# Performance work log

Measured on AMD Instinct MI355X. Metric: run time of the kernel, lower is better.

## Reference

```python
import jax, jax.numpy as jnp
import numpy as np

B, C, H, W = 64, 3, 512, 512


def setup_inputs() -> dict:
    key = jax.random.key(0)
    return {"segmentation_mask": jax.random.normal(key, (B, C, H, W), dtype=jnp.float32)}


def _vertical_height(pred_mask, label):
    # pred_mask: (B, H, W) int. Returns (B, 1) float32 = ymax - ymin for rows
    # containing `label`, or 0 if the label is absent (matches the torch loop
    # which leaves bounds at zeros).
    row_any = (pred_mask == label).any(axis=2)          # (B, H) bool
    has = row_any.any(axis=1)                            # (B,)
    Hdim = row_any.shape[1]
    ymin = jnp.argmax(row_any, axis=1)                   # first True row
    ymax = Hdim - 1 - jnp.argmax(row_any[:, ::-1], axis=1)  # last True row
    height = jnp.where(has, (ymax - ymin).astype(jnp.float32), 0.0)
    return height[:, None]                               # (B, 1)


def reference(segmentation_mask):
    pred_mask = jnp.argmax(segmentation_mask, axis=1)    # (B, H, W)

    cup_height = _vertical_height(pred_mask, 1)          # (B, 1)
    disc_height = _vertical_height(pred_mask, 2)         # (B, 1)
    cdr = cup_height / (disc_height + 1e-6)              # (B, 1)

    prob_map = jax.nn.softmax(segmentation_mask, axis=1) # (B, 3, H, W)
    cup_prob = prob_map[:, 1]                            # (B, H, W)
    disc_prob = prob_map[:, 2]

    # AdaptiveAvgPool2d(1)+Flatten on a (B,1,H,W) map == global spatial mean,
    # identical to .mean(dim=(1,2)); the original concatenates both, so the
    # disc/cup means appear twice.
    disc_mean = disc_prob.mean(axis=(1, 2))[:, None]     # (B, 1)
    cup_mean = cup_prob.mean(axis=(1, 2))[:, None]       # (B, 1)

    return jnp.concatenate([cdr, disc_mean, cup_mean, disc_mean, cup_mean], axis=1)  # (B, 5)
```

## Files before the change

### kernel.cpp

```cpp
#include <hip/hip_runtime.h>
#include <hip/hip_bf16.h>
#include <math.h>


#define BATCH 64
#define CHAN 3
#define HDIM 512
#define WDIM 512
#define HW (HDIM * WDIM)
#define RPB 8
#define THREADS 256
#define VECS_PER_ROW (WDIM / 4)
#define NV (RPB * VECS_PER_ROW)
#define ITERS (NV / THREADS)
#define NBLOCKS (BATCH * (HDIM / RPB))

typedef float vfloat4 __attribute__((ext_vector_type(4)));

struct Accum {
    int ymax1[BATCH];
    int yminenc1[BATCH];
    int ymax2[BATCH];
    int yminenc2[BATCH];
    float sum1[BATCH];
    float sum2[BATCH];
};

__global__ __launch_bounds__(THREADS) void cdr_main(const float* __restrict__ in,
                                                    Accum* __restrict__ acc) {
    const int b = blockIdx.x >> 6;
    const int chunk = blockIdx.x & 63;
    const int row0 = chunk * RPB;

    const vfloat4* __restrict__ c0 =
        (const vfloat4*)(in + (size_t)b * CHAN * HW + (size_t)row0 * WDIM);
    const vfloat4* __restrict__ c1 = c0 + (HW / 4);
    const vfloat4* __restrict__ c2 = c1 + (HW / 4);

    vfloat4 va[ITERS], vb[ITERS], vc[ITERS];
#pragma unroll
    for (int j = 0; j < ITERS; ++j) {
        const int v = threadIdx.x + j * THREADS;
        va[j] = __builtin_nontemporal_load(&c0[v]);
        vb[j] = __builtin_nontemporal_load(&c1[v]);
        vc[j] = __builtin_nontemporal_load(&c2[v]);
    }

    float acc1 = 0.0f, acc2 = 0.0f;
    unsigned m = 0u;
    const int rbase = threadIdx.x >> 7;

#pragma unroll
    for (int j = 0; j < ITERS; ++j) {
        unsigned f1 = 0u, f2 = 0u;

#define DO_PX(V0, V1, V2)                                        \
        {                                                        \
            f1 |= (unsigned)(((V1) > (V0)) & ((V1) >= (V2)));    \
            f2 |= (unsigned)(((V2) > (V0)) & ((V2) > (V1)));     \
            float e0 = __expf(V0);                               \
            float e1 = __expf(V1);                               \
            float e2 = __expf(V2);                               \
            float inv = __builtin_amdgcn_rcpf(e0 + e1 + e2);     \
            acc1 += e1 * inv;                                    \
            acc2 += e2 * inv;                                    \
        }

        DO_PX(va[j].x, vb[j].x, vc[j].x)
        DO_PX(va[j].y, vb[j].y, vc[j].y)
        DO_PX(va[j].z, vb[j].z, vc[j].z)
        DO_PX(va[j].w, vb[j].w, vc[j].w)
#undef DO_PX

        const int row = rbase + 2 * j;
        m |= (f1 << row) | (f2 << (16 + row));
    }

#pragma unroll
    for (int off = 32; off > 0; off >>= 1) {
        m |= __shfl_xor(m, off, 64);
        acc1 += __shfl_down(acc1, off, 64);
        acc2 += __shfl_down(acc2, off, 64);
    }

    __shared__ unsigned s_m[THREADS / 64];
    __shared__ float s_red1[THREADS / 64];
    __shared__ float s_red2[THREADS / 64];
    const int wave = threadIdx.x >> 6;
    if ((threadIdx.x & 63) == 0) {
        s_m[wave] = m;
        s_red1[wave] = acc1;
        s_red2[wave] = acc2;
    }
    __syncthreads();

    if (threadIdx.x == 0) {
        float t1 = 0.0f, t2 = 0.0f;
        unsigned mm = 0u;
        for (int w = 0; w < THREADS / 64; ++w) {
            t1 += s_red1[w];
            t2 += s_red2[w];
            mm |= s_m[w];
        }
        atomicAdd(&acc->sum1[b], t1);
        atomicAdd(&acc->sum2[b], t2);

        const unsigned bm1 = mm & 0xFFu;
        const unsigned bm2 = (mm >> 16) & 0xFFu;
        if (bm1) {
            const int bmin = row0 + (__ffs(bm1) - 1);
            const int bmax = row0 + (31 - __clz(bm1));
            atomicMax(&acc->ymax1[b], bmax);
            atomicMax(&acc->yminenc1[b], (HDIM - 1) - bmin);
        }
        if (bm2) {
            const int bmin = row0 + (__ffs(bm2) - 1);
            const int bmax = row0 + (31 - __clz(bm2));
            atomicMax(&acc->ymax2[b], bmax);
            atomicMax(&acc->yminenc2[b], (HDIM - 1) - bmin);
        }
    }
}

__global__ void cdr_finalize(const Accum* __restrict__ acc, float* __restrict__ out) {
    const int b = threadIdx.x;
    if (b < BATCH) {
        const int ymax1 = acc->ymax1[b];
        const int ymax2 = acc->ymax2[b];
        const int ymin1 = (HDIM - 1) - acc->yminenc1[b];
        const int ymin2 = (HDIM - 1) - acc->yminenc2[b];
        float h1 = (ymax1 >= 0) ? (float)(ymax1 - ymin1) : 0.0f;
        float h2 = (ymax2 >= 0) ? (float)(ymax2 - ymin2) : 0.0f;
        float cdr = h1 / (h2 + 1e-6f);
        const float inv_hw = 1.0f / (float)HW;
        float cup_mean = acc->sum1[b] * inv_hw;
        float disc_mean = acc->sum2[b] * inv_hw;
        out[b * 5 + 0] = cdr;
        out[b * 5 + 1] = disc_mean;
        out[b * 5 + 2] = cup_mean;
        out[b * 5 + 3] = disc_mean;
        out[b * 5 + 4] = cup_mean;
    }
}

extern "C" void kernel_launch(void* const* d_in, const int* in_sizes, int n_in,
                              void* d_out, int out_size, void* d_ws, size_t ws_size,
                              hipStream_t stream) {
    const float* in = (const float*)d_in[0];
    float* out = (float*)d_out;
    Accum* acc = (Accum*)d_ws;

    cdr_main<<<NBLOCKS, THREADS, 0, stream>>>(in, acc);
    cdr_finalize<<<1, 64, 0, stream>>>(acc, out);
}
```

Before: 266.7 us.

## Double-buffer register loads across row chunks with larger per-block work

Each block now covers 32 rows instead of 8, processed as four chunks with a register double buffer that prefetches the next chunk while computing the current one. Row masks for the two labels are split into separate 32-bit words. This aims to overlap memory latency with exp/compare work and to reduce block count and atomic traffic. It raises register pressure and lowers the number of blocks, which may hurt occupancy and latency hiding.

```diff
diff --git a/kernel.cpp b/kernel.cpp
--- a/kernel.cpp
+++ b/kernel.cpp
@@ -8,12 +8,11 @@
 #define HDIM 512
 #define WDIM 512
 #define HW (HDIM * WDIM)
-#define RPB 8
 #define THREADS 256
-#define VECS_PER_ROW (WDIM / 4)
-#define NV (RPB * VECS_PER_ROW)
-#define ITERS (NV / THREADS)
-#define NBLOCKS (BATCH * (HDIM / RPB))
+#define CHUNKS 4
+#define BLOCKS_PER_IMG 16
+#define NBLOCKS (BATCH * BLOCKS_PER_IMG)
+#define CHUNK_V 1024
 
 typedef float vfloat4 __attribute__((ext_vector_type(4)));
 
@@ -28,67 +27,82 @@
 
 __global__ __launch_bounds__(THREADS) void cdr_main(const float* __restrict__ in,
                                                     Accum* __restrict__ acc) {
-    const int b = blockIdx.x >> 6;
-    const int chunk = blockIdx.x & 63;
-    const int row0 = chunk * RPB;
+    const int b = blockIdx.x >> 4;
+    const int part = blockIdx.x & 15;
+    const int row0 = part * 32;
 
     const vfloat4* __restrict__ c0 =
         (const vfloat4*)(in + (size_t)b * CHAN * HW + (size_t)row0 * WDIM);
     const vfloat4* __restrict__ c1 = c0 + (HW / 4);
     const vfloat4* __restrict__ c2 = c1 + (HW / 4);
 
-    vfloat4 va[ITERS], vb[ITERS], vc[ITERS];
+    vfloat4 A[2][3][4];
+
+    auto load_chunk = [&](int c, int buf) {
 #pragma unroll
-    for (int j = 0; j < ITERS; ++j) {
-        const int v = threadIdx.x + j * THREADS;
-        va[j] = __builtin_nontemporal_load(&c0[v]);
-        vb[j] = __builtin_nontemporal_load(&c1[v]);
-        vc[j] = __builtin_nontemporal_load(&c2[v]);
-    }
+        for (int j = 0; j < 4; ++j) {
+            const int v = c * CHUNK_V + j * THREADS + (int)threadIdx.x;
+            A[buf][0][j] = __builtin_nontemporal_load(&c0[v]);
+            A[buf][1][j] = __builtin_nontemporal_load(&c1[v]);
+            A[buf][2][j] = __builtin_nontemporal_load(&c2[v]);
+        }
+    };
+
+    load_chunk(0, 0);
 
     float acc1 = 0.0f, acc2 = 0.0f;
-    unsigned m = 0u;
+    unsigned m1 = 0u, m2 = 0u;
     const int rbase = threadIdx.x >> 7;
 
 #pragma unroll
-    for (int j = 0; j < ITERS; ++j) {
-        unsigned f1 = 0u, f2 = 0u;
+    for (int c = 0; c < CHUNKS; ++c) {
+        const int buf = c & 1;
+        if (c < CHUNKS - 1) load_chunk(c + 1, buf ^ 1);
+
+#pragma unroll
+        for (int j = 0; j < 4; ++j) {
+            unsigned f1 = 0u, f2 = 0u;
 
 #define DO_PX(V0, V1, V2)                                        \
-        {                                                        \
-            f1 |= (unsigned)(((V1) > (V0)) & ((V1) >= (V2)));    \
-            f2 |= (unsigned)(((V2) > (V0)) & ((V2) > (V1)));     \
-            float e0 = __expf(V0);                               \
-            float e1 = __expf(V1);                               \
-            float e2 = __expf(V2);                               \
-            float inv = __builtin_amdgcn_rcpf(e0 + e1 + e2);     \
-            acc1 += e1 * inv;                                    \
-            acc2 += e2 * inv;                                    \
-        }
+            {                                                    \
+                f1 |= (unsigned)(((V1) > (V0)) & ((V1) >= (V2)));\
+                f2 |= (unsigned)(((V2) > (V0)) & ((V2) > (V1))); \
+                float e0 = __expf(V0);                           \
+                float e1 = __expf(V1);                           \
+                float e2 = __expf(V2);                           \
+                float inv = __builtin_amdgcn_rcpf(e0 + e1 + e2); \
+                acc1 += e1 * inv;                                \
+                acc2 += e2 * inv;                                \
+            }
 
-        DO_PX(va[j].x, vb[j].x, vc[j].x)
-        DO_PX(va[j].y, vb[j].y, vc[j].y)
-        DO_PX(va[j].z, vb[j].z, vc[j].z)
-        DO_PX(va[j].w, vb[j].w, vc[j].w)
+            DO_PX(A[buf][0][j].x, A[buf][1][j].x, A[buf][2][j].x)
+            DO_PX(A[buf][0][j].y, A[buf][1][j].y, A[buf][2][j].y)
+            DO_PX(A[buf][0][j].z, A[buf][1][j].z, A[buf][2][j].z)
+            DO_PX(A[buf][0][j].w, A[buf][1][j].w, A[buf][2][j].w)
 #undef DO_PX
 
-        const int row = rbase + 2 * j;
-        m |= (f1 << row) | (f2 << (16 + row));
+            const int bit = c * 8 + 2 * j + rbase;
+            m1 |= f1 << bit;
+            m2 |= f2 << bit;
+        }
     }
 
 #pragma unroll
     for (int off = 32; off > 0; off >>= 1) {
-        m |= __shfl_xor(m, off, 64);
+        m1 |= __shfl_xor(m1, off, 64);
+        m2 |= __shfl_xor(m2, off, 64);
         acc1 += __shfl_down(acc1, off, 64);
         acc2 += __shfl_down(acc2, off, 64);
     }
 
-    __shared__ unsigned s_m[THREADS / 64];
+    __shared__ unsigned s_m1[THREADS / 64];
+    __shared__ unsigned s_m2[THREADS / 64];
     __shared__ float s_red1[THREADS / 64];
     __shared__ float s_red2[THREADS / 64];
     const int wave = threadIdx.x >> 6;
     if ((threadIdx.x & 63) == 0) {
-        s_m[wave] = m;
+        s_m1[wave] = m1;
+        s_m2[wave] = m2;
         s_red1[wave] = acc1;
         s_red2[wave] = acc2;
     }
@@ -96,26 +110,25 @@
 
     if (threadIdx.x == 0) {
         float t1 = 0.0f, t2 = 0.0f;
-        unsigned mm = 0u;
+        unsigned mm1 = 0u, mm2 = 0u;
         for (int w = 0; w < THREADS / 64; ++w) {
             t1 += s_red1[w];
             t2 += s_red2[w];
-            mm |= s_m[w];
+            mm1 |= s_m1[w];
+            mm2 |= s_m2[w];
         }
         atomicAdd(&acc->sum1[b], t1);
         atomicAdd(&acc->sum2[b], t2);
 
-        const unsigned bm1 = mm & 0xFFu;
-        const unsigned bm2 = (mm >> 16) & 0xFFu;
-        if (bm1) {
-            const int bmin = row0 + (__ffs(bm1) - 1);
-            const int bmax = row0 + (31 - __clz(bm1));
+        if (mm1) {
+            const int bmin = row0 + (__ffs(mm1) - 1);
+            const int bmax = row0 + (31 - __clz(mm1));
             atomicMax(&acc->ymax1[b], bmax);
             atomicMax(&acc->yminenc1[b], (HDIM - 1) - bmin);
         }
-        if (bm2) {
-            const int bmin = row0 + (__ffs(bm2) - 1);
-            const int bmax = row0 + (31 - __clz(bm2));
+        if (mm2) {
+            const int bmin = row0 + (__ffs(mm2) - 1);
+            const int bmax = row0 + (31 - __clz(mm2));
             atomicMax(&acc->ymax2[b], bmax);
             atomicMax(&acc->yminenc2[b], (HDIM - 1) - bmin);
         }
```

Result: faster. 250.5 us (-6.1%).
